# Optimization experiments

Hardware: AMD Instinct MI355X
Metric: run time of the kernel (lower is better)

Reference implementation:

```python
import jax, jax.numpy as jnp
import numpy as np
import math

B, T, C, H = 2, 2048, 1024, 16
HD = C // H  # head dim = 64

def setup_inputs() -> dict:
    key = jax.random.key(0)
    ks = jax.random.split(key, 12)
    s = 0.02
    return {
        "x": jax.random.normal(ks[0], (B, T, C), dtype=jnp.float32),
        "ln1_g": jnp.ones((C,), jnp.float32),
        "ln1_b": jnp.zeros((C,), jnp.float32),
        "W_attn": jax.random.normal(ks[1], (C, 3 * C), jnp.float32) * s,
        "b_attn": jnp.zeros((3 * C,), jnp.float32),
        "W_ap": jax.random.normal(ks[2], (C, C), jnp.float32) * s,
        "b_ap": jnp.zeros((C,), jnp.float32),
        "ln2_g": jnp.ones((C,), jnp.float32),
        "ln2_b": jnp.zeros((C,), jnp.float32),
        "W_fc": jax.random.normal(ks[3], (C, 4 * C), jnp.float32) * s,
        "b_fc": jnp.zeros((4 * C,), jnp.float32),
        "W_mp": jax.random.normal(ks[4], (4 * C, C), jnp.float32) * s,
        "b_mp": jnp.zeros((C,), jnp.float32),
    }

def layernorm(x, g, b, eps=1e-5):
    mu = jnp.mean(x, axis=-1, keepdims=True)
    var = jnp.mean(jnp.square(x - mu), axis=-1, keepdims=True)
    return (x - mu) * jax.lax.rsqrt(var + eps) * g + b

def gelu_tanh(x):
    # GELU(approximate='tanh')
    c = math.sqrt(2.0 / math.pi)
    return 0.5 * x * (1.0 + jnp.tanh(c * (x + 0.044715 * x * x * x)))

def attention(x, W_attn, b_attn, W_ap, b_ap):
    b, t, c = x.shape
    qkv = x @ W_attn + b_attn                      # [B,T,3C]
    q, k, v = jnp.split(qkv, 3, axis=-1)
    q = q.reshape(b, t, H, HD).transpose(0, 2, 1, 3)  # [B,H,T,hd]
    k = k.reshape(b, t, H, HD).transpose(0, 2, 1, 3)
    v = v.reshape(b, t, H, HD).transpose(0, 2, 1, 3)
    attn = jnp.einsum('bhqd,bhkd->bhqk', q, k) * (1.0 / math.sqrt(HD))
    mask = jnp.tril(jnp.ones((t, t), dtype=bool))
    attn = jnp.where(mask, attn, jnp.float32(-jnp.inf))
    attn = jax.nn.softmax(attn, axis=-1)
    y = jnp.einsum('bhqk,bhkd->bhqd', attn, v)
    y = y.transpose(0, 2, 1, 3).reshape(b, t, c)
    return y @ W_ap + b_ap

def reference(x, ln1_g, ln1_b, W_attn, b_attn, W_ap, b_ap,
              ln2_g, ln2_b, W_fc, b_fc, W_mp, b_mp):
    x = x + attention(layernorm(x, ln1_g, ln1_b), W_attn, b_attn, W_ap, b_ap)
    h = layernorm(x, ln2_g, ln2_b)
    h = gelu_tanh(h @ W_fc + b_fc) @ W_mp + b_mp
    return x + h
```

## Files before the change

kernel.cpp:

```cpp
#include <hip/hip_runtime.h>
#include <stdint.h>

#define TT_ 2048
#define CC_ 1024

typedef unsigned short u16;
typedef __bf16 bf16x8 __attribute__((ext_vector_type(8)));
typedef float f32x4 __attribute__((ext_vector_type(4)));
typedef unsigned short u16x8 __attribute__((ext_vector_type(8)));
typedef unsigned int u32x2 __attribute__((ext_vector_type(2)));

__device__ __forceinline__ u16 f2bf(float f) {
  unsigned u = __float_as_uint(f);
  u += 0x7fff + ((u >> 16) & 1);
  return (u16)(u >> 16);
}
__device__ __forceinline__ float bf2f(u16 v) {
  return __uint_as_float(((unsigned)v) << 16);
}

__device__ __forceinline__ float gelu_f(float t) {
  float u = 1.5957691216057308f * (t + 0.044715f * t * t * t);
  return t / (1.f + __expf(-u));
}

__device__ __forceinline__ void async_cp16(const u16* g, u16* l) {
  __builtin_amdgcn_global_load_lds(
      (const __attribute__((address_space(1))) void*)(uintptr_t)g,
      (__attribute__((address_space(3))) void*)(uint32_t)(uintptr_t)l,
      16, 0, 0);
}

__device__ __forceinline__ void blockbar() {
  asm volatile("" ::: "memory");
  __builtin_amdgcn_s_barrier();
  asm volatile("" ::: "memory");
}

__global__ __launch_bounds__(256) void kconv_t(const float* __restrict__ W,
                                               u16* __restrict__ WT, int K, int N) {
  __shared__ float t[32][33];
  int n0 = blockIdx.x * 32, k0 = blockIdx.y * 32;
  int tx = threadIdx.x & 31, ty = threadIdx.x >> 5;
#pragma unroll
  for (int r = 0; r < 4; ++r)
    t[ty + 8 * r][tx] = W[(size_t)(k0 + ty + 8 * r) * N + n0 + tx];
  __syncthreads();
#pragma unroll
  for (int r = 0; r < 4; ++r)
    WT[(size_t)(n0 + ty + 8 * r) * K + k0 + tx] = f2bf(t[tx][ty + 8 * r]);
}

__global__ __launch_bounds__(256) void kln(const float* __restrict__ x,
                                           const float* __restrict__ g,
                                           const float* __restrict__ b,
                                           u16* __restrict__ out) {
  int row = blockIdx.x, tid = threadIdx.x;
  const float4* xr = (const float4*)(x + (size_t)row * CC_);
  float4 v = xr[tid];
  float s = v.x + v.y + v.z + v.w;
  float s2 = v.x * v.x + v.y * v.y + v.z * v.z + v.w * v.w;
#pragma unroll
  for (int off = 32; off; off >>= 1) { s += __shfl_down(s, off); s2 += __shfl_down(s2, off); }
  __shared__ float rs[4], rq[4];
  int w = tid >> 6;
  if ((tid & 63) == 0) { rs[w] = s; rq[w] = s2; }
  __syncthreads();
  s = rs[0] + rs[1] + rs[2] + rs[3];
  s2 = rq[0] + rq[1] + rq[2] + rq[3];
  float mean = s * (1.f / CC_);
  float var = s2 * (1.f / CC_) - mean * mean;
  float rstd = rsqrtf(var + 1e-5f);
  float4 gv = ((const float4*)g)[tid];
  float4 bv = ((const float4*)b)[tid];
  u16* orow = out + (size_t)row * CC_ + tid * 4;
  orow[0] = f2bf((v.x - mean) * rstd * gv.x + bv.x);
  orow[1] = f2bf((v.y - mean) * rstd * gv.y + bv.y);
  orow[2] = f2bf((v.z - mean) * rstd * gv.z + bv.z);
  orow[3] = f2bf((v.w - mean) * rstd * gv.w + bv.w);
}

template <int EPI, int NSPLIT>
__global__ __launch_bounds__(256) void kgemm(const u16* __restrict__ A,
                                             const u16* __restrict__ BTm,
                                             const float* __restrict__ bias,
                                             const float* __restrict__ resid,
                                             void* __restrict__ out,
                                             float* __restrict__ part,
                                             int M, int N, int Ktot) {
  __shared__ __align__(16) u16 As[2][128 * 32];
  __shared__ __align__(16) u16 Bs[2][128 * 32];
  const int tid = threadIdx.x, lane = tid & 63, w = tid >> 6;
  const int llo = lane & 15, lhi = lane >> 4;
  const int row0 = blockIdx.y * 128, col0 = blockIdx.x * 128;
  const int wr = w >> 1, wc = w & 1;
  const int crow = lane >> 2;
  const int ck = (lane & 3) * 8;
  const int Kc = Ktot / NSPLIT;
  const int klo = (NSPLIT > 1) ? blockIdx.z * Kc : 0;

  f32x4 acc[4][4] = {};

  auto stage = [&](int bufi, int kof) {
#pragma unroll
    for (int c = w; c < 8; c += 4) {
      int r = c * 16 + crow;
      async_cp16(A + (size_t)(row0 + r) * Ktot + klo + kof + ck, &As[bufi][c * 512]);
      async_cp16(BTm + (size_t)(col0 + r) * Ktot + klo + kof + ck, &Bs[bufi][c * 512]);
    }
  };

  const int nt = Kc / 32;
  stage(0, 0);
  asm volatile("s_waitcnt vmcnt(0)" ::: "memory");
  blockbar();
  int cur = 0;

  for (int t = 0; t < nt; ++t) {
    if (t + 1 < nt) stage(cur ^ 1, (t + 1) * 32);
    bf16x8 af[4], bfr[4];
#pragma unroll
    for (int m = 0; m < 4; ++m)
      af[m] = *(const bf16x8*)&As[cur][(wr * 64 + m * 16 + llo) * 32 + lhi * 8];
#pragma unroll
    for (int n = 0; n < 4; ++n)
      bfr[n] = *(const bf16x8*)&Bs[cur][(wc * 64 + n * 16 + llo) * 32 + lhi * 8];
#pragma unroll
    for (int m = 0; m < 4; ++m)
#pragma unroll
      for (int n = 0; n < 4; ++n)
        acc[m][n] = __builtin_amdgcn_mfma_f32_16x16x32_bf16(af[m], bfr[n], acc[m][n], 0, 0, 0);
    if (t + 1 < nt) {
      asm volatile("s_waitcnt vmcnt(0)" ::: "memory");
      blockbar();
    }
    cur ^= 1;
  }

  const int c_row = row0 + wr * 64 + lhi * 4;
  const int c_col = col0 + wc * 64 + llo;
  const bool fin = (NSPLIT == 1) || (blockIdx.z == 0);
#pragma unroll
  for (int n = 0; n < 4; ++n) {
    int col = c_col + n * 16;
    float bb = bias[col];
#pragma unroll
    for (int m = 0; m < 4; ++m) {
      f32x4 a = acc[m][n];
#pragma unroll
      for (int i = 0; i < 4; ++i) {
        size_t idx = (size_t)(c_row + m * 16 + i) * N + col;
        if (!fin) {
          part[idx] = a[i];
        } else {
          float val = a[i] + bb;
          if constexpr (EPI == 1) {
            ((float*)out)[idx] = val + resid[idx];
          } else if constexpr (EPI == 2) {
            ((u16*)out)[idx] = f2bf(gelu_f(val));
          } else {
            ((u16*)out)[idx] = f2bf(val);
          }
        }
      }
    }
  }
}

__global__ __launch_bounds__(256) void kadd(float* __restrict__ out,
                                            const float* __restrict__ part) {
  size_t i = ((size_t)blockIdx.x * 256 + threadIdx.x) * 4;
  float4 o = *(float4*)(out + i);
  float4 p = *(const float4*)(part + i);
  o.x += p.x; o.y += p.y; o.z += p.z; o.w += p.w;
  *(float4*)(out + i) = o;
}

__global__ __launch_bounds__(256) void kvtrans(const u16* __restrict__ qkv,
                                               u16* __restrict__ VT) {
  int tt = blockIdx.x;
  int bh = blockIdx.y;
  int b = bh >> 4, h = bh & 15;
  __shared__ u16 t[64][72];
  int r = threadIdx.x >> 3, c0 = (threadIdx.x & 7) * 8;
  const u16* src = qkv + (size_t)(b * TT_ + tt * 64) * 3072 + 2048 + h * 64;
#pragma unroll
  for (int it = 0; it < 2; ++it) {
    int rr = r + it * 32;
    *(u16x8*)&t[rr][c0] = *(const u16x8*)(src + (size_t)rr * 3072 + c0);
  }
  __syncthreads();
  u16* dst = VT + ((size_t)bh * 64) * TT_ + tt * 64;
#pragma unroll
  for (int it = 0; it < 2; ++it) {
    int d = r + it * 32;
    u16x8 v;
#pragma unroll
    for (int e = 0; e < 8; ++e) v[e] = t[c0 + e][d];
    *(u16x8*)(dst + (size_t)d * TT_ + c0) = v;
  }
}

__global__ __launch_bounds__(512, 4) void kattn(const u16* __restrict__ qkv,
                                                const u16* __restrict__ VT,
                                                u16* __restrict__ y) {
  const int h = blockIdx.x, b = blockIdx.y;
  const int z = blockIdx.z;
  const int qt = (z < 8) ? (15 - z) : (z - 8);
  const int tid = threadIdx.x, lane = tid & 63, w = tid >> 6;
  const int llo = lane & 15, lhi = lane >> 4;

  __shared__ __align__(16) u16 Qs[128 * 64];
  __shared__ __align__(16) u16 Ks[2][64 * 64];
  __shared__ __align__(16) u16 Vs[2][64 * 64];
  __shared__ __align__(16) u16 Ps[128 * 72];

  const size_t tok0 = (size_t)b * TT_;
  const int q0 = qt * 128;
  const u16* qb = qkv + tok0 * 3072 + h * 64;
  const u16* kb = qb + 1024;

  {
    const float alpha = 0.18033688011112042f;
    int r8 = tid >> 3, ce = (tid & 7) * 8;
#pragma unroll
    for (int it = 0; it < 2; ++it) {
      int tk = it * 64 + r8;
      u16x8 v = *(const u16x8*)(qb + (size_t)(q0 + tk) * 3072 + ce);
#pragma unroll
      for (int e = 0; e < 8; ++e) v[e] = f2bf(bf2f(v[e]) * alpha);
      *(u16x8*)&Qs[tk * 64 + (ce ^ ((tk & 7) << 3))] = v;
    }
  }
  asm volatile("s_waitcnt lgkmcnt(0)" ::: "memory");

  const int p_ = w * 8 + (lane >> 3);
  const int krow = ((p_ & 15) << 2) | (p_ >> 4);
  const int scol = ((lane & 7) * 8) ^ ((p_ & 7) << 3);
  const u16* kg = kb + (size_t)krow * 3072 + scol;
  const u16* vg = VT + ((size_t)(b * 16 + h) * 64 + p_) * TT_ + scol;

  const int ntiles = 2 * qt + 2;
  async_cp16(kg, &Ks[0][w * 512]);
  async_cp16(vg, &Vs[0][w * 512]);

  blockbar();

  bf16x8 aq[2];
#pragma unroll
  for (int kk = 0; kk < 2; ++kk)
    aq[kk] = *(const bf16x8*)&Qs[(w * 16 + llo) * 64 + ((kk * 32 + lhi * 8) ^ ((llo & 7) << 3))];

  float m_i[4], l_i[4];
  f32x4 o[4] = {};
#pragma unroll
  for (int i = 0; i < 4; ++i) { m_i[i] = -1e30f; l_i[i] = 0.f; }

  const int row_min = q0 + w * 16, row_max = row_min + 15;
  int buf = 0;

  for (int j = 0; j < ntiles; ++j) {
    if (j + 1 < ntiles) {
      async_cp16(kg + (size_t)(j + 1) * (64 * 3072), &Ks[buf ^ 1][w * 512]);
      async_cp16(vg + (size_t)(j + 1) * 64, &Vs[buf ^ 1][w * 512]);
      asm volatile("s_waitcnt vmcnt(2)" ::: "memory");
    } else {
      asm volatile("s_waitcnt vmcnt(0)" ::: "memory");
    }
    blockbar();

    const int kmin = j * 64;
    if (kmin <= row_max) {
      f32x4 s[4] = {};
      __builtin_amdgcn_s_setprio(1);
#pragma unroll
      for (int nb = 0; nb < 4; ++nb)
#pragma unroll
        for (int kk = 0; kk < 2; ++kk) {
          bf16x8 bk = *(const bf16x8*)&Ks[buf][(nb * 16 + llo) * 64 +
                                              ((kk * 32 + lhi * 8) ^ ((llo & 7) << 3))];
          s[nb] = __builtin_amdgcn_mfma_f32_16x16x32_bf16(aq[kk], bk, s[nb], 0, 0, 0);
        }
      __builtin_amdgcn_s_setprio(0);

      const bool part = (kmin + 63 > row_min);
      float sc[4][4];
#pragma unroll
      for (int nb = 0; nb < 4; ++nb)
#pragma unroll
        for (int i = 0; i < 4; ++i) {
          float v = s[nb][i];
          if (part && (kmin + llo * 4 + nb > row_min + lhi * 4 + i)) v = -1e30f;
          sc[nb][i] = v;
        }

      float rm[4];
#pragma unroll
      for (int i = 0; i < 4; ++i) {
        float r = fmaxf(fmaxf(sc[0][i], sc[1][i]), fmaxf(sc[2][i], sc[3][i]));
#pragma unroll
        for (int off = 1; off < 16; off <<= 1) r = fmaxf(r, __shfl_xor(r, off));
        rm[i] = r;
      }

      bool need = (rm[0] > m_i[0] + 8.f) | (rm[1] > m_i[1] + 8.f) |
                  (rm[2] > m_i[2] + 8.f) | (rm[3] > m_i[3] + 8.f);
      if (__any(need)) {
#pragma unroll
        for (int i = 0; i < 4; ++i) {
          float mn = fmaxf(m_i[i], rm[i]);
          float corr = exp2f(m_i[i] - mn);
          l_i[i] *= corr;
#pragma unroll
          for (int db = 0; db < 4; ++db) o[db][i] *= corr;
          m_i[i] = mn;
        }
      }

#pragma unroll
      for (int i = 0; i < 4; ++i) {
        float p0 = exp2f(sc[0][i] - m_i[i]);
        float p1 = exp2f(sc[1][i] - m_i[i]);
        float p2 = exp2f(sc[2][i] - m_i[i]);
        float p3 = exp2f(sc[3][i] - m_i[i]);
        float rsum = (p0 + p1) + (p2 + p3);
#pragma unroll
        for (int off = 1; off < 16; off <<= 1) rsum += __shfl_xor(rsum, off);
        l_i[i] += rsum;
        u32x2 pk;
        pk[0] = (unsigned)f2bf(p0) | ((unsigned)f2bf(p1) << 16);
        pk[1] = (unsigned)f2bf(p2) | ((unsigned)f2bf(p3) << 16);
        *(u32x2*)&Ps[(w * 16 + lhi * 4 + i) * 72 + llo * 4] = pk;
      }

      bf16x8 pa[2];
#pragma unroll
      for (int kk = 0; kk < 2; ++kk)
        pa[kk] = *(const bf16x8*)&Ps[(w * 16 + llo) * 72 + kk * 32 + lhi * 8];
      __builtin_amdgcn_s_setprio(1);
#pragma unroll
      for (int db = 0; db < 4; ++db)
#pragma unroll
        for (int kk = 0; kk < 2; ++kk) {
          bf16x8 bv = *(const bf16x8*)&Vs[buf][(db * 16 + llo) * 64 +
                                              ((kk * 32 + lhi * 8) ^ ((llo & 7) << 3))];
          o[db] = __builtin_amdgcn_mfma_f32_16x16x32_bf16(pa[kk], bv, o[db], 0, 0, 0);
        }
      __builtin_amdgcn_s_setprio(0);
    }
    blockbar();
    buf ^= 1;
  }

#pragma unroll
  for (int i = 0; i < 4; ++i) {
    float inv = 1.f / l_i[i];
    size_t row = tok0 + q0 + w * 16 + lhi * 4 + i;
#pragma unroll
    for (int db = 0; db < 4; ++db)
      y[row * CC_ + h * 64 + db * 16 + llo] = f2bf(o[db][i] * inv);
  }
}

extern "C" void kernel_launch(void* const* d_in, const int* in_sizes, int n_in,
                              void* d_out, int out_size, void* d_ws, size_t ws_size,
                              hipStream_t stream) {
  (void)in_sizes; (void)n_in; (void)out_size; (void)ws_size;
  const float* x      = (const float*)d_in[0];
  const float* ln1g   = (const float*)d_in[1];
  const float* ln1b   = (const float*)d_in[2];
  const float* W_attn = (const float*)d_in[3];
  const float* b_attn = (const float*)d_in[4];
  const float* W_ap   = (const float*)d_in[5];
  const float* b_ap   = (const float*)d_in[6];
  const float* ln2g   = (const float*)d_in[7];
  const float* ln2b   = (const float*)d_in[8];
  const float* W_fc   = (const float*)d_in[9];
  const float* b_fc   = (const float*)d_in[10];
  const float* W_mp   = (const float*)d_in[11];
  const float* b_mp   = (const float*)d_in[12];

  char* p = (char*)d_ws;
  u16* WTattn = (u16*)p; p += (size_t)3072 * 1024 * 2;
  u16* WTap   = (u16*)p; p += (size_t)1024 * 1024 * 2;
  u16* WTfc   = (u16*)p; p += (size_t)4096 * 1024 * 2;
  u16* WTmp   = (u16*)p; p += (size_t)4096 * 1024 * 2;
  u16* xn     = (u16*)p; p += (size_t)4096 * 1024 * 2;
  u16* qkvb   = (u16*)p; p += (size_t)4096 * 3072 * 2;
  u16* yb     = (u16*)p; p += (size_t)4096 * 1024 * 2;
  float* x1   = (float*)p; p += (size_t)4096 * 1024 * 4;
  u16* h2     = (u16*)p; p += (size_t)4096 * 1024 * 2;
  u16* fcb    = qkvb;
  u16* VT     = (u16*)x1;
  float* mppart = (float*)d_ws;

  kconv_t<<<dim3(96, 32), 256, 0, stream>>>(W_attn, WTattn, 1024, 3072);
  kconv_t<<<dim3(32, 32), 256, 0, stream>>>(W_ap, WTap, 1024, 1024);
  kconv_t<<<dim3(128, 32), 256, 0, stream>>>(W_fc, WTfc, 1024, 4096);
  kconv_t<<<dim3(32, 128), 256, 0, stream>>>(W_mp, WTmp, 4096, 1024);

  kln<<<4096, 256, 0, stream>>>(x, ln1g, ln1b, xn);
  kgemm<0, 1><<<dim3(24, 32), 256, 0, stream>>>(xn, WTattn, b_attn, nullptr, qkvb, nullptr, 4096, 3072, 1024);
  kvtrans<<<dim3(32, 32), 256, 0, stream>>>(qkvb, VT);
  kattn<<<dim3(16, 2, 16), 512, 0, stream>>>(qkvb, VT, yb);
  kgemm<1, 1><<<dim3(8, 32), 256, 0, stream>>>(yb, WTap, b_ap, x, x1, nullptr, 4096, 1024, 1024);
  kln<<<4096, 256, 0, stream>>>(x1, ln2g, ln2b, h2);
  kgemm<2, 1><<<dim3(32, 32), 256, 0, stream>>>(h2, WTfc, b_fc, nullptr, fcb, nullptr, 4096, 4096, 1024);
  kgemm<1, 2><<<dim3(8, 32, 2), 256, 0, stream>>>(fcb, WTmp, b_mp, x1, (float*)d_out, mppart, 4096, 1024, 4096);
  kadd<<<4096, 256, 0, stream>>>((float*)d_out, mppart);
}
```

Measured before the change: 279.4 us.

## Add 256x256-tile 512-thread GEMM with 4-stage async pipeline for QKV, FC, MLP-proj

Introduces a new GEMM kernel using 256x256 block tiles, 8 waves, a 4-slot async LDS pipeline with swizzled layout, and uses it for the QKV, FC and MLP projection GEMMs. The MLP projection now uses split-K of 4 with bf16 partial sums reduced by a new kadd3 kernel, and the workspace is reordered so partials overwrite the no-longer-needed W_attn buffer. Larger tiles raise data reuse per block, while storing partials in bf16 halves the reduction traffic at some precision cost. The bigger tiles give fewer blocks (192–256), which may underfill the GPU's CUs.

```diff
diff --git a/kernel.cpp b/kernel.cpp
--- a/kernel.cpp
+++ b/kernel.cpp
@@ -167,13 +167,128 @@
   }
 }
 
-__global__ __launch_bounds__(256) void kadd(float* __restrict__ out,
-                                            const float* __restrict__ part) {
-  size_t i = ((size_t)blockIdx.x * 256 + threadIdx.x) * 4;
-  float4 o = *(float4*)(out + i);
-  float4 p = *(const float4*)(part + i);
-  o.x += p.x; o.y += p.y; o.z += p.z; o.w += p.w;
-  *(float4*)(out + i) = o;
+template <int EPI, int NSPLIT>
+__global__ __launch_bounds__(512, 2) void kgemm2(const u16* __restrict__ A,
+                                                 const u16* __restrict__ BTm,
+                                                 const float* __restrict__ bias,
+                                                 const float* __restrict__ resid,
+                                                 void* __restrict__ out,
+                                                 u16* __restrict__ part,
+                                                 int M, int N, int Ktot) {
+  __shared__ __align__(16) u16 LB[4][2][8192];
+  const int tid = threadIdx.x, lane = tid & 63, w = tid >> 6;
+  const int llo = lane & 15, lhi = lane >> 4;
+  const int wr = w >> 2, wc = w & 3;
+  const int row0 = blockIdx.y * 256, col0 = blockIdx.x * 256;
+  const int Kc = Ktot / NSPLIT;
+  const int klo = (NSPLIT > 1) ? blockIdx.z * Kc : 0;
+  const int nt = Kc / 32;
+
+  const int wsA = w & 3;
+  const int hbB = (wc >> 1);
+  const int wsB = (w & 1) + ((w >> 2) << 1);
+
+  const u16 *gA[2], *gB[2];
+  int ldsA[2], ldsB[2];
+#pragma unroll
+  for (int l = 0; l < 2; ++l) {
+    int c = l * 256 + wsA * 64 + lane;
+    int rowl = c >> 2;
+    int kc = ((c & 3) ^ ((c >> 3) & 3)) * 8;
+    gA[l] = A + (size_t)(row0 + wr * 128 + rowl) * Ktot + klo + kc;
+    ldsA[l] = wr * 4096 + (l * 256 + wsA * 64) * 8;
+    int c2 = l * 256 + wsB * 64 + lane;
+    int row2 = c2 >> 2;
+    int kc2 = ((c2 & 3) ^ ((c2 >> 3) & 3)) * 8;
+    gB[l] = BTm + (size_t)(col0 + hbB * 128 + row2) * Ktot + klo + kc2;
+    ldsB[l] = hbB * 4096 + (l * 256 + wsB * 64) * 8;
+  }
+
+  auto stage = [&](int t) {
+    int slot = t & 3;
+#pragma unroll
+    for (int l = 0; l < 2; ++l) {
+      async_cp16(gA[l] + (size_t)t * 32, &LB[slot][0][ldsA[l]]);
+      async_cp16(gB[l] + (size_t)t * 32, &LB[slot][1][ldsB[l]]);
+    }
+  };
+
+  f32x4 acc[8][4] = {};
+  for (int t = 0; t < 3 && t < nt; ++t) stage(t);
+  const int swz = (llo >> 1) & 3;
+  const int aoffb = wr * 4096 + llo * 32 + (lhi ^ swz) * 8;
+  const int boffb = hbB * 4096 + ((wc & 1) * 64 + llo) * 32 + (lhi ^ swz) * 8;
+
+  for (int t = 0; t < nt; ++t) {
+    const int slot = t & 3;
+    const int rem = nt - 1 - t;
+    if (rem >= 2)      asm volatile("s_waitcnt vmcnt(8)" ::: "memory");
+    else if (rem == 1) asm volatile("s_waitcnt vmcnt(4)" ::: "memory");
+    else               asm volatile("s_waitcnt vmcnt(0)" ::: "memory");
+    asm volatile("s_waitcnt lgkmcnt(0)" ::: "memory");
+    blockbar();
+    if (t + 3 < nt) stage(t + 3);
+
+    bf16x8 af[8], bfv[4];
+#pragma unroll
+    for (int n = 0; n < 4; ++n)
+      bfv[n] = *(const bf16x8*)&LB[slot][1][boffb + n * 512];
+#pragma unroll
+    for (int m = 0; m < 8; ++m)
+      af[m] = *(const bf16x8*)&LB[slot][0][aoffb + m * 512];
+    __builtin_amdgcn_s_setprio(1);
+#pragma unroll
+    for (int m = 0; m < 8; ++m)
+#pragma unroll
+      for (int n = 0; n < 4; ++n)
+        acc[m][n] = __builtin_amdgcn_mfma_f32_16x16x32_bf16(af[m], bfv[n], acc[m][n], 0, 0, 0);
+    __builtin_amdgcn_s_setprio(0);
+  }
+
+  const int c_row0 = row0 + wr * 128 + lhi * 4;
+  const int c_col0 = col0 + wc * 64 + llo;
+  const bool fin = (NSPLIT == 1) || (blockIdx.z == 0);
+  u16* pb = part + (NSPLIT > 1 ? ((size_t)(blockIdx.z - 1)) * M * N : 0);
+#pragma unroll
+  for (int n = 0; n < 4; ++n) {
+    int col = c_col0 + n * 16;
+    float bb = bias[col];
+#pragma unroll
+    for (int m = 0; m < 8; ++m) {
+      f32x4 a = acc[m][n];
+#pragma unroll
+      for (int i = 0; i < 4; ++i) {
+        size_t idx = (size_t)(c_row0 + m * 16 + i) * N + col;
+        if (!fin) {
+          pb[idx] = f2bf(a[i]);
+        } else {
+          float val = a[i] + bb;
+          if constexpr (EPI == 1) {
+            ((float*)out)[idx] = val + resid[idx];
+          } else if constexpr (EPI == 2) {
+            ((u16*)out)[idx] = f2bf(gelu_f(val));
+          } else {
+            ((u16*)out)[idx] = f2bf(val);
+          }
+        }
+      }
+    }
+  }
+}
+
+__global__ __launch_bounds__(256) void kadd3(float* __restrict__ out,
+                                             const u16* __restrict__ p, size_t MN) {
+  size_t i0 = ((size_t)blockIdx.x * 256 + threadIdx.x) * 8;
+  float4 o0 = *(float4*)(out + i0);
+  float4 o1 = *(float4*)(out + i0 + 4);
+#pragma unroll
+  for (int s = 0; s < 3; ++s) {
+    u16x8 v = *(const u16x8*)(p + s * MN + i0);
+    o0.x += bf2f(v[0]); o0.y += bf2f(v[1]); o0.z += bf2f(v[2]); o0.w += bf2f(v[3]);
+    o1.x += bf2f(v[4]); o1.y += bf2f(v[5]); o1.z += bf2f(v[6]); o1.w += bf2f(v[7]);
+  }
+  *(float4*)(out + i0) = o0;
+  *(float4*)(out + i0 + 4) = o1;
 }
 
 __global__ __launch_bounds__(256) void kvtrans(const u16* __restrict__ qkv,
@@ -381,10 +496,10 @@
   const float* b_mp   = (const float*)d_in[12];
 
   char* p = (char*)d_ws;
+  u16* WTmp   = (u16*)p; p += (size_t)4096 * 1024 * 2;
   u16* WTattn = (u16*)p; p += (size_t)3072 * 1024 * 2;
   u16* WTap   = (u16*)p; p += (size_t)1024 * 1024 * 2;
   u16* WTfc   = (u16*)p; p += (size_t)4096 * 1024 * 2;
-  u16* WTmp   = (u16*)p; p += (size_t)4096 * 1024 * 2;
   u16* xn     = (u16*)p; p += (size_t)4096 * 1024 * 2;
   u16* qkvb   = (u16*)p; p += (size_t)4096 * 3072 * 2;
   u16* yb     = (u16*)p; p += (size_t)4096 * 1024 * 2;
@@ -392,7 +507,7 @@
   u16* h2     = (u16*)p; p += (size_t)4096 * 1024 * 2;
   u16* fcb    = qkvb;
   u16* VT     = (u16*)x1;
-  float* mppart = (float*)d_ws;
+  u16* mpp    = WTattn;
 
   kconv_t<<<dim3(96, 32), 256, 0, stream>>>(W_attn, WTattn, 1024, 3072);
   kconv_t<<<dim3(32, 32), 256, 0, stream>>>(W_ap, WTap, 1024, 1024);
@@ -400,12 +515,12 @@
   kconv_t<<<dim3(32, 128), 256, 0, stream>>>(W_mp, WTmp, 4096, 1024);
 
   kln<<<4096, 256, 0, stream>>>(x, ln1g, ln1b, xn);
-  kgemm<0, 1><<<dim3(24, 32), 256, 0, stream>>>(xn, WTattn, b_attn, nullptr, qkvb, nullptr, 4096, 3072, 1024);
+  kgemm2<0, 1><<<dim3(12, 16), 512, 0, stream>>>(xn, WTattn, b_attn, nullptr, qkvb, nullptr, 4096, 3072, 1024);
   kvtrans<<<dim3(32, 32), 256, 0, stream>>>(qkvb, VT);
   kattn<<<dim3(16, 2, 16), 512, 0, stream>>>(qkvb, VT, yb);
   kgemm<1, 1><<<dim3(8, 32), 256, 0, stream>>>(yb, WTap, b_ap, x, x1, nullptr, 4096, 1024, 1024);
   kln<<<4096, 256, 0, stream>>>(x1, ln2g, ln2b, h2);
-  kgemm<2, 1><<<dim3(32, 32), 256, 0, stream>>>(h2, WTfc, b_fc, nullptr, fcb, nullptr, 4096, 4096, 1024);
-  kgemm<1, 2><<<dim3(8, 32, 2), 256, 0, stream>>>(fcb, WTmp, b_mp, x1, (float*)d_out, mppart, 4096, 1024, 4096);
-  kadd<<<4096, 256, 0, stream>>>((float*)d_out, mppart);
-}
+  kgemm2<2, 1><<<dim3(16, 16), 512, 0, stream>>>(h2, WTfc, b_fc, nullptr, fcb, nullptr, 4096, 4096, 1024);
+  kgemm2<1, 4><<<dim3(4, 16, 4), 512, 0, stream>>>(fcb, WTmp, b_mp, x1, (float*)d_out, mpp, 4096, 1024, 4096);
+  kadd3<<<2048, 256, 0, stream>>>((float*)d_out, mpp, (size_t)4096 * 1024);
+}
```

Measured after the change: 283.0 us. About the same (+1.3%).
